# Performance work log

Measured on AMD Instinct MI355X. Metric: run time of the kernel, lower is better.

Reference implementation:

```python
import jax, jax.numpy as jnp
import numpy as np

B, T, C = 2, 4096, 2048
HS = 64
DW, DA, DV, DG = 128, 128, 64, 224


def setup_inputs() -> dict:
    key = jax.random.key(0)
    ks = jax.random.split(key, 32)
    s = 0.02  # small weight scale to keep activations in a sane range
    inp = {
        'x': jax.random.normal(ks[0], (B, T, C), jnp.float32),
        'v_first': jax.random.normal(ks[1], (B, T, C), jnp.float32),
        'x_r': jax.random.uniform(ks[2], (C,), jnp.float32),
        'x_w': jax.random.uniform(ks[3], (C,), jnp.float32),
        'x_k': jax.random.uniform(ks[4], (C,), jnp.float32),
        'x_v': jax.random.uniform(ks[5], (C,), jnp.float32),
        'x_a': jax.random.uniform(ks[6], (C,), jnp.float32),
        'x_g': jax.random.uniform(ks[7], (C,), jnp.float32),
        'w0': jax.random.normal(ks[8], (C,), jnp.float32),
        'w1': jax.random.normal(ks[9], (C, DW), jnp.float32) * s,
        'w2': jax.random.normal(ks[10], (DW, C), jnp.float32) * s,
        'a0': jax.random.normal(ks[11], (C,), jnp.float32),
        'a1': jax.random.normal(ks[12], (C, DA), jnp.float32) * s,
        'a2': jax.random.normal(ks[13], (DA, C), jnp.float32) * s,
        'v0': jax.random.normal(ks[14], (C,), jnp.float32),
        'v1': jax.random.normal(ks[15], (C, DV), jnp.float32) * s,
        'v2': jax.random.normal(ks[16], (DV, C), jnp.float32) * s,
        'g1': jax.random.normal(ks[17], (C, DG), jnp.float32) * s,
        'g2': jax.random.normal(ks[18], (DG, C), jnp.float32) * s,
        'k_k': jax.random.normal(ks[19], (C,), jnp.float32) * 0.1 + 0.71,
        'k_a': jnp.full((C,), 1.02, jnp.float32),
        'Wr': jax.random.normal(ks[20], (C, C), jnp.float32) * s,
        'Wk': jax.random.normal(ks[21], (C, C), jnp.float32) * s,
        'Wv': jax.random.normal(ks[22], (C, C), jnp.float32) * s,
        'head_size': HS,
    }
    return inp


def reference(x, v_first, x_r, x_w, x_k, x_v, x_a, x_g,
              w0, w1, w2, a0, a1, a2, v0, v1, v2, g1, g2,
              k_k, k_a, Wr, Wk, Wv, head_size):
    Bd, Td, Cd = x.shape
    H = Cd // head_size
    # time shift: prepend zero frame, drop last
    xprev = jnp.concatenate([jnp.zeros_like(x[:, :1]), x[:, :-1]], axis=1)
    xx = xprev - x
    xr = x + xx * x_r
    xw = x + xx * x_w
    xk = x + xx * x_k
    xv = x + xx * x_v
    xa = x + xx * x_a
    xg = x + xx * x_g
    r = xr @ Wr.T                                   # [B,T,C]
    w = -jax.nn.softplus(-(w0 + jnp.tanh(xw @ w1) @ w2)) - 0.5
    k = xk @ Wk.T
    v = xv @ Wv.T
    # layer_id = 1 != 0  ->  mix with v_first
    v = v + (v_first - v) * jax.nn.sigmoid(v0 + (xv @ v1) @ v2)
    a = jax.nn.sigmoid(a0 + (xa @ a1) @ a2)
    g = jax.nn.sigmoid(xg @ g1) @ g2
    kk = k * k_k
    kk4 = kk.reshape(Bd, Td, H, head_size)
    nrm = jnp.linalg.norm(kk4, axis=-1, keepdims=True)
    kk = (kk4 / jnp.maximum(nrm, 1e-12)).reshape(Bd, Td, Cd)
    k = k * (1.0 + (a - 1.0) * k_a)
    return (r, w, k, v, a, g, kk, v_first)
```

## Files before the change

### kernel.cpp

```cpp
#include <hip/hip_runtime.h>
#include <hip/hip_bf16.h>

#define MTOT 8192
#define TLEN 4096
#define CDIM 2048
#define SLOT ((size_t)MTOT * CDIM)

typedef __attribute__((ext_vector_type(4))) float f32x4;
typedef __attribute__((ext_vector_type(8))) __bf16 bf16x8;

__device__ __forceinline__ short f2bf(float f) {
  __hip_bfloat16 h = __float2bfloat16(f);
  return __builtin_bit_cast(short, h);
}

__device__ __forceinline__ float sigm(float x) { return 1.f / (1.f + expf(-x)); }

__device__ __forceinline__ void gload16(const void* g, void* l) {
  __builtin_amdgcn_global_load_lds(
      (__attribute__((address_space(1))) void*)g,
      (__attribute__((address_space(3))) void*)l, 16, 0, 0);
}

__device__ __forceinline__ void gemm_core(
    const short* __restrict__ A, int lda,
    const short* __restrict__ Bt, int ldb,
    int K, int m0, int n0,
    short* As, short* Bs, f32x4 acc[4][4])
{
  const int tid  = threadIdx.x;
  const int lane = tid & 63;
  const int wv   = tid >> 6;
  const int wy   = wv >> 1;
  const int wx   = wv & 1;
  const int quad = lane >> 4;
  const int m16  = lane & 15;

  const f32x4 zero = {0.f, 0.f, 0.f, 0.f};
  #pragma unroll
  for (int i = 0; i < 4; ++i)
    #pragma unroll
    for (int j = 0; j < 4; ++j)
      acc[i][j] = zero;

  const int e0 = (wv * 64 + lane) * 8;
  const int e1 = e0 + 2048;
  const int r0 = e0 >> 5, c0 = e0 & 31;
  const int r1 = e1 >> 5, c1 = e1 & 31;
  const int lb0 = wv * 512;
  const int lb1 = 2048 + wv * 512;

  const short* pa0 = A  + (size_t)(m0 + r0) * lda + c0;
  const short* pa1 = A  + (size_t)(m0 + r1) * lda + c1;
  const short* pb0 = Bt + (size_t)(n0 + r0) * ldb + c0;
  const short* pb1 = Bt + (size_t)(n0 + r1) * ldb + c1;

  for (int k0 = 0; k0 < K; k0 += 32) {
    gload16(pa0 + k0, As + lb0);
    gload16(pa1 + k0, As + lb1);
    gload16(pb0 + k0, Bs + lb0);
    gload16(pb1 + k0, Bs + lb1);
    __syncthreads();

    bf16x8 af[4], bfr[4];
    #pragma unroll
    for (int mi = 0; mi < 4; ++mi)
      af[mi] = *(const bf16x8*)(As + (wy*64 + mi*16 + m16)*32 + quad*8);
    #pragma unroll
    for (int ni = 0; ni < 4; ++ni)
      bfr[ni] = *(const bf16x8*)(Bs + (wx*64 + ni*16 + m16)*32 + quad*8);

    #pragma unroll
    for (int mi = 0; mi < 4; ++mi)
      #pragma unroll
      for (int ni = 0; ni < 4; ++ni)
        acc[mi][ni] = __builtin_amdgcn_mfma_f32_16x16x32_bf16(
            af[mi], bfr[ni], acc[mi][ni], 0, 0, 0);
    __syncthreads();
  }
}

__global__ __launch_bounds__(256) void mix_kernel(
    const float* __restrict__ x, const float* __restrict__ vfin,
    const float* __restrict__ cr, const float* __restrict__ cw,
    const float* __restrict__ ck, const float* __restrict__ cv,
    const float* __restrict__ ca, const float* __restrict__ cg,
    short* __restrict__ xr, short* __restrict__ xw, short* __restrict__ xk,
    short* __restrict__ xv, short* __restrict__ xa, short* __restrict__ xg,
    float* __restrict__ vfout)
{
  const size_t i = (size_t)blockIdx.x * 256 + threadIdx.x;
  const size_t e = i * 4;
  const int c = (int)(e & (CDIM - 1));
  const size_t m = e >> 11;
  const int t = (int)(m & (TLEN - 1));
  const float4 xc = *(const float4*)(x + e);
  float4 xp = make_float4(0.f, 0.f, 0.f, 0.f);
  if (t > 0) xp = *(const float4*)(x + e - CDIM);
  const float d0 = xp.x - xc.x, d1 = xp.y - xc.y;
  const float d2 = xp.z - xc.z, d3 = xp.w - xc.w;

  *(float4*)(vfout + e) = *(const float4*)(vfin + e);

  #define EMIT(coef, dst) { \
    const float4 cf = *(const float4*)((coef) + c); \
    short4 s; \
    s.x = f2bf(xc.x + d0 * cf.x); \
    s.y = f2bf(xc.y + d1 * cf.y); \
    s.z = f2bf(xc.z + d2 * cf.z); \
    s.w = f2bf(xc.w + d3 * cf.w); \
    *(short4*)((dst) + e) = s; }
  EMIT(cr, xr) EMIT(cw, xw) EMIT(ck, xk) EMIT(cv, xv) EMIT(ca, xa) EMIT(cg, xg)
  #undef EMIT
}

__global__ __launch_bounds__(256) void cvt_big(
    const float* __restrict__ Wr, const float* __restrict__ Wk,
    const float* __restrict__ Wv,
    short* __restrict__ br, short* __restrict__ bk, short* __restrict__ bv)
{
  const int z = blockIdx.y;
  const float* src = (z == 0) ? Wr : (z == 1) ? Wk : Wv;
  short* dst = (z == 0) ? br : (z == 1) ? bk : bv;
  const size_t e = ((size_t)blockIdx.x * 256 + threadIdx.x) * 4;
  const float4 v = *(const float4*)(src + e);
  short4 s;
  s.x = f2bf(v.x); s.y = f2bf(v.y); s.z = f2bf(v.z); s.w = f2bf(v.w);
  *(short4*)(dst + e) = s;
}

__global__ __launch_bounds__(256) void wtrans(
    const float* __restrict__ w1, const float* __restrict__ a1,
    const float* __restrict__ v1, const float* __restrict__ g1,
    const float* __restrict__ w2, const float* __restrict__ a2,
    const float* __restrict__ v2, const float* __restrict__ g2,
    short* __restrict__ w1t, short* __restrict__ a1t,
    short* __restrict__ v1t, short* __restrict__ g1t,
    short* __restrict__ w2t, short* __restrict__ a2t,
    short* __restrict__ v2t, short* __restrict__ g2t)
{
  const int task = blockIdx.y;
  const int i = blockIdx.x * 256 + threadIdx.x;
  switch (task) {
    case 0: if (i < 128*2048) { int d=i>>11, c=i&2047; w1t[i]=f2bf(w1[(size_t)c*128+d]); } break;
    case 1: if (i < 128*2048) { int d=i>>11, c=i&2047; a1t[i]=f2bf(a1[(size_t)c*128+d]); } break;
    case 2: if (i < 128*2048) { int d=i>>11, c=i&2047; v1t[i]=(d<64)?f2bf(v1[(size_t)c*64+d]):(short)0; } break;
    case 3: if (i < 256*2048) { int d=i>>11, c=i&2047; g1t[i]=(d<224)?f2bf(g1[(size_t)c*224+d]):(short)0; } break;
    case 4: if (i < 2048*128) { int c=i>>7, d=i&127; w2t[i]=f2bf(w2[(size_t)d*2048+c]); } break;
    case 5: if (i < 2048*128) { int c=i>>7, d=i&127; a2t[i]=f2bf(a2[(size_t)d*2048+c]); } break;
    case 6: if (i < 2048*64)  { int c=i>>6, d=i&63;  v2t[i]=f2bf(v2[(size_t)d*2048+c]); } break;
    case 7: if (i < 2048*224) { int c=i/224, d=i-c*224; g2t[i]=f2bf(g2[(size_t)d*2048+c]); } break;
  }
}

__global__ __launch_bounds__(512, 2) void gemm_big2(
    const short* __restrict__ xr, const short* __restrict__ xk,
    const short* __restrict__ xv,
    const short* __restrict__ Wr, const short* __restrict__ Wk,
    const short* __restrict__ Wv,
    float* __restrict__ out)
{
  __shared__ short As[32768];
  __shared__ short Bs[32768];

  const int z = blockIdx.z;
  const short* A  = (z == 0) ? xr : (z == 1) ? xk : xv;
  const short* Bt = (z == 0) ? Wr : (z == 1) ? Wk : Wv;
  float* O = (z == 0) ? out : (z == 1) ? out + 2*SLOT : out + 3*SLOT;

  const int m0 = blockIdx.x * 256, n0 = blockIdx.y * 256;
  const int tid  = threadIdx.x;
  const int lane = tid & 63, wid = tid >> 6;
  const int wm = wid >> 2, wn = wid & 3;
  const int quad = lane >> 4, m16 = lane & 15;

  const int srow = tid >> 2;
  const int csrc = (((tid & 3) ^ ((tid >> 3) & 3)) << 3);
  const size_t aoff = (size_t)(m0 + srow) * CDIM + csrc;
  const size_t boff = (size_t)(n0 + srow) * CDIM + csrc;
  const int lbase = wid * 512;

  const int fslot = ((quad ^ ((m16 >> 1) & 3)) << 3);
  const int abase = (wm*128 + m16) * 32 + fslot;
  const int bbase = (wn*64  + m16) * 32 + fslot;

  f32x4 acc[8][4];
  const f32x4 zf = {0.f, 0.f, 0.f, 0.f};
  #pragma unroll
  for (int i = 0; i < 8; ++i)
    #pragma unroll
    for (int j = 0; j < 4; ++j) acc[i][j] = zf;

  #define STG(REG, BASEP, OFF, KOFF) do { \
    gload16((BASEP) + (OFF) + (KOFF), (REG) + lbase); \
    gload16((BASEP) + (OFF) + (KOFF) + (size_t)128*CDIM, (REG) + lbase + 4096); \
  } while (0)

  STG(As + 0,    A,  aoff, 0);
  STG(Bs + 0,    Bt, boff, 0);
  STG(As + 8192, A,  aoff, 32);
  STG(Bs + 8192, Bt, boff, 32);
  asm volatile("s_waitcnt vmcnt(4)" ::: "memory");
  __builtin_amdgcn_s_barrier();
  __builtin_amdgcn_sched_barrier(0);

  const int NT = CDIM / 64;
  for (int t = 0; t < NT; ++t) {
    const int db = (t & 1) << 14;
    const int nb = 16384 - db;
    const int kn = t*64 + 64;
    const bool pf = (kn < CDIM);
    short* Ar0 = As + db;
    short* Br0 = Bs + db;
    short* Ar1 = As + db + 8192;
    short* Br1 = Bs + db + 8192;

    bf16x8 af[8], b0, b1;

    #pragma unroll
    for (int mi = 0; mi < 8; ++mi)
      af[mi] = *(const bf16x8*)(Ar0 + abase + mi*512);
    b0 = *(const bf16x8*)(Br0 + bbase + 0*512);
    b1 = *(const bf16x8*)(Br0 + bbase + 1*512);
    if (pf) STG(As + nb, A, aoff, kn);
    __builtin_amdgcn_s_barrier();
    asm volatile("s_waitcnt lgkmcnt(0)" ::: "memory");
    __builtin_amdgcn_sched_barrier(0);
    __builtin_amdgcn_s_setprio(1);
    #pragma unroll
    for (int mi = 0; mi < 8; ++mi)
      acc[mi][0] = __builtin_amdgcn_mfma_f32_16x16x32_bf16(af[mi], b0, acc[mi][0], 0, 0, 0);
    #pragma unroll
    for (int mi = 0; mi < 8; ++mi)
      acc[mi][1] = __builtin_amdgcn_mfma_f32_16x16x32_bf16(af[mi], b1, acc[mi][1], 0, 0, 0);
    __builtin_amdgcn_s_setprio(0);
    __builtin_amdgcn_s_barrier();

    b0 = *(const bf16x8*)(Br0 + bbase + 2*512);
    b1 = *(const bf16x8*)(Br0 + bbase + 3*512);
    if (pf) STG(Bs + nb, Bt, boff, kn);
    __builtin_amdgcn_s_barrier();
    asm volatile("s_waitcnt lgkmcnt(0)" ::: "memory");
    __builtin_amdgcn_sched_barrier(0);
    __builtin_amdgcn_s_setprio(1);
    #pragma unroll
    for (int mi = 0; mi < 8; ++mi)
      acc[mi][2] = __builtin_amdgcn_mfma_f32_16x16x32_bf16(af[mi], b0, acc[mi][2], 0, 0, 0);
    #pragma unroll
    for (int mi = 0; mi < 8; ++mi)
      acc[mi][3] = __builtin_amdgcn_mfma_f32_16x16x32_bf16(af[mi], b1, acc[mi][3], 0, 0, 0);
    __builtin_amdgcn_s_setprio(0);
    if (pf) asm volatile("s_waitcnt vmcnt(4)" ::: "memory");
    else    asm volatile("s_waitcnt vmcnt(0)" ::: "memory");
    __builtin_amdgcn_s_barrier();
    __builtin_amdgcn_sched_barrier(0);

    #pragma unroll
    for (int mi = 0; mi < 8; ++mi)
      af[mi] = *(const bf16x8*)(Ar1 + abase + mi*512);
    b0 = *(const bf16x8*)(Br1 + bbase + 0*512);
    b1 = *(const bf16x8*)(Br1 + bbase + 1*512);
    if (pf) STG(As + nb + 8192, A, aoff, kn + 32);
    __builtin_amdgcn_s_barrier();
    asm volatile("s_waitcnt lgkmcnt(0)" ::: "memory");
    __builtin_amdgcn_sched_barrier(0);
    __builtin_amdgcn_s_setprio(1);
    #pragma unroll
    for (int mi = 0; mi < 8; ++mi)
      acc[mi][0] = __builtin_amdgcn_mfma_f32_16x16x32_bf16(af[mi], b0, acc[mi][0], 0, 0, 0);
    #pragma unroll
    for (int mi = 0; mi < 8; ++mi)
      acc[mi][1] = __builtin_amdgcn_mfma_f32_16x16x32_bf16(af[mi], b1, acc[mi][1], 0, 0, 0);
    __builtin_amdgcn_s_setprio(0);
    __builtin_amdgcn_s_barrier();

    b0 = *(const bf16x8*)(Br1 + bbase + 2*512);
    b1 = *(const bf16x8*)(Br1 + bbase + 3*512);
    if (pf) STG(Bs + nb + 8192, Bt, boff, kn + 32);
    __builtin_amdgcn_s_barrier();
    asm volatile("s_waitcnt lgkmcnt(0)" ::: "memory");
    __builtin_amdgcn_sched_barrier(0);
    __builtin_amdgcn_s_setprio(1);
    #pragma unroll
    for (int mi = 0; mi < 8; ++mi)
      acc[mi][2] = __builtin_amdgcn_mfma_f32_16x16x32_bf16(af[mi], b0, acc[mi][2], 0, 0, 0);
    #pragma unroll
    for (int mi = 0; mi < 8; ++mi)
      acc[mi][3] = __builtin_amdgcn_mfma_f32_16x16x32_bf16(af[mi], b1, acc[mi][3], 0, 0, 0);
    __builtin_amdgcn_s_setprio(0);
    asm volatile("s_waitcnt vmcnt(4)" ::: "memory");
    __builtin_amdgcn_s_barrier();
    __builtin_amdgcn_sched_barrier(0);
  }
  #undef STG

  #pragma unroll
  for (int mi = 0; mi < 8; ++mi) {
    const int row = m0 + wm*128 + mi*16 + quad*4;
    #pragma unroll
    for (int ni = 0; ni < 4; ++ni) {
      const int col = n0 + wn*64 + ni*16 + m16;
      #pragma unroll
      for (int r = 0; r < 4; ++r)
        O[(size_t)(row + r) * CDIM + col] = acc[mi][ni][r];
    }
  }
}

__global__ __launch_bounds__(256) void gemm_s1(
    const short* __restrict__ xw, const short* __restrict__ xa,
    const short* __restrict__ xv, const short* __restrict__ xg,
    const short* __restrict__ w1t, const short* __restrict__ a1t,
    const short* __restrict__ v1t, const short* __restrict__ g1t,
    short* __restrict__ hw, short* __restrict__ ha,
    short* __restrict__ hv, short* __restrict__ hg)
{
  const int z = blockIdx.z;
  const int nb = blockIdx.y;
  if (z != 3 && nb != 0) return;
  __shared__ short As[4096], Bs[4096];
  const short* A  = (z==0) ? xw  : (z==1) ? xa  : (z==2) ? xv  : xg;
  const short* Bt = (z==0) ? w1t : (z==1) ? a1t : (z==2) ? v1t : g1t;
  short* H        = (z==0) ? hw  : (z==1) ? ha  : (z==2) ? hv  : hg;
  const int Nreal = (z==2) ? 64 : (z==3) ? 224 : 128;
  const int m0 = blockIdx.x * 128, n0 = nb * 128;
  f32x4 acc[4][4];
  gemm_core(A, CDIM, Bt, CDIM, CDIM, m0, n0, As, Bs, acc);

  const int tid=threadIdx.x, lane=tid&63, wv=tid>>6;
  const int wy=wv>>1, wx=wv&1, quad=lane>>4, m16=lane&15;
  #pragma unroll
  for (int mi = 0; mi < 4; ++mi) {
    const int mb = m0 + wy*64 + mi*16 + quad*4;
    #pragma unroll
    for (int ni = 0; ni < 4; ++ni) {
      const int n = n0 + wx*64 + ni*16 + m16;
      if (n < Nreal) {
        #pragma unroll
        for (int r = 0; r < 4; ++r) {
          float v = acc[mi][ni][r];
          if (z == 0) v = tanhf(v);
          else if (z == 3) v = sigm(v);
          H[(size_t)(mb + r) * Nreal + n] = f2bf(v);
        }
      }
    }
  }
}

__global__ __launch_bounds__(256) void gemm_s2(
    const short* __restrict__ hw, const short* __restrict__ ha,
    const short* __restrict__ hv, const short* __restrict__ hg,
    const short* __restrict__ w2t, const short* __restrict__ a2t,
    const short* __restrict__ v2t, const short* __restrict__ g2t,
    const float* __restrict__ w0, const float* __restrict__ a0,
    const float* __restrict__ v0, const float* __restrict__ vfirst,
    float* __restrict__ out)
{
  __shared__ short As[4096], Bs[4096];
  const int z = blockIdx.z;
  const short* A  = (z==0) ? hw  : (z==1) ? ha  : (z==2) ? hv  : hg;
  const short* Bt = (z==0) ? w2t : (z==1) ? a2t : (z==2) ? v2t : g2t;
  const int K = (z==2) ? 64 : (z==3) ? 224 : 128;
  const int m0 = blockIdx.x * 128, n0 = blockIdx.y * 128;
  f32x4 acc[4][4];
  gemm_core(A, K, Bt, K, K, m0, n0, As, Bs, acc);

  const int tid=threadIdx.x, lane=tid&63, wv=tid>>6;
  const int wy=wv>>1, wx=wv&1, quad=lane>>4, m16=lane&15;
  #pragma unroll
  for (int mi = 0; mi < 4; ++mi) {
    const int mb = m0 + wy*64 + mi*16 + quad*4;
    #pragma unroll
    for (int ni = 0; ni < 4; ++ni) {
      const int n = n0 + wx*64 + ni*16 + m16;
      #pragma unroll
      for (int r = 0; r < 4; ++r) {
        const float val = acc[mi][ni][r];
        const size_t idx = (size_t)(mb + r) * CDIM + n;
        if (z == 0) {
          float zz = w0[n] + val;
          float sp = fmaxf(-zz, 0.f) + log1pf(expf(-fabsf(zz)));
          out[SLOT + idx] = -sp - 0.5f;
        } else if (z == 1) {
          out[4*SLOT + idx] = sigm(a0[n] + val);
        } else if (z == 2) {
          const float gate = sigm(v0[n] + val);
          const float vr = out[3*SLOT + idx];
          out[3*SLOT + idx] = vr + (vfirst[idx] - vr) * gate;
        } else {
          out[5*SLOT + idx] = val;
        }
      }
    }
  }
}

__global__ __launch_bounds__(256) void fin_k(
    const float* __restrict__ kkc, const float* __restrict__ kac,
    float* __restrict__ out)
{
  const int wid  = blockIdx.x * 4 + (threadIdx.x >> 6);
  const int lane = threadIdx.x & 63;
  const size_t m = (size_t)(wid >> 5);
  const int h = wid & 31;
  const int c = h * 64 + lane;
  const size_t idx = m * CDIM + c;
  const float kraw = out[2*SLOT + idx];
  const float a    = out[4*SLOT + idx];
  const float kkv  = kraw * kkc[c];
  float ss = kkv * kkv;
  #pragma unroll
  for (int o = 32; o >= 1; o >>= 1) ss += __shfl_xor(ss, o, 64);
  const float nrm = sqrtf(ss);
  out[6*SLOT + idx] = kkv / fmaxf(nrm, 1e-12f);
  out[2*SLOT + idx] = kraw * (1.f + (a - 1.f) * kac[c]);
}

extern "C" void kernel_launch(void* const* d_in, const int* in_sizes, int n_in,
                              void* d_out, int out_size, void* d_ws, size_t ws_size,
                              hipStream_t stream) {
  (void)in_sizes; (void)n_in; (void)out_size; (void)ws_size;
  const float* x   = (const float*)d_in[0];
  const float* vf  = (const float*)d_in[1];
  const float* x_r = (const float*)d_in[2];
  const float* x_w = (const float*)d_in[3];
  const float* x_k = (const float*)d_in[4];
  const float* x_v = (const float*)d_in[5];
  const float* x_a = (const float*)d_in[6];
  const float* x_g = (const float*)d_in[7];
  const float* w0  = (const float*)d_in[8];
  const float* w1  = (const float*)d_in[9];
  const float* w2  = (const float*)d_in[10];
  const float* a0  = (const float*)d_in[11];
  const float* a1  = (const float*)d_in[12];
  const float* a2  = (const float*)d_in[13];
  const float* v0  = (const float*)d_in[14];
  const float* v1  = (const float*)d_in[15];
  const float* v2  = (const float*)d_in[16];
  const float* g1  = (const float*)d_in[17];
  const float* g2  = (const float*)d_in[18];
  const float* k_k = (const float*)d_in[19];
  const float* k_a = (const float*)d_in[20];
  const float* Wr  = (const float*)d_in[21];
  const float* Wk  = (const float*)d_in[22];
  const float* Wv  = (const float*)d_in[23];

  float* out = (float*)d_out;

  short* xr_b = (short*)(out + 1*SLOT);
  short* xw_b = xr_b + SLOT;
  short* xk_b = (short*)(out + 4*SLOT);
  short* xv_b = xk_b + SLOT;
  short* xa_b = (short*)(out + 5*SLOT);
  short* xg_b = xa_b + SLOT;

  char* wsp = (char*)d_ws;
  size_t off = 0;
  #define ALLOC(var, bytes) short* var = (short*)(wsp + off); off += (((size_t)(bytes)) + 255) & ~(size_t)255;
  ALLOC(Wr_b, (size_t)CDIM*CDIM*2)
  ALLOC(Wk_b, (size_t)CDIM*CDIM*2)
  ALLOC(Wv_b, (size_t)CDIM*CDIM*2)
  ALLOC(w1t, 128*2048*2)
  ALLOC(a1t, 128*2048*2)
  ALLOC(v1t, 128*2048*2)
  ALLOC(g1t, 256*2048*2)
  ALLOC(w2t, 2048*128*2)
  ALLOC(a2t, 2048*128*2)
  ALLOC(v2t, 2048*64*2)
  ALLOC(g2t, 2048*224*2)
  ALLOC(hw, (size_t)MTOT*128*2)
  ALLOC(ha, (size_t)MTOT*128*2)
  ALLOC(hv, (size_t)MTOT*64*2)
  ALLOC(hg, (size_t)MTOT*224*2)
  #undef ALLOC

  mix_kernel<<<dim3(16384), 256, 0, stream>>>(
      x, vf, x_r, x_w, x_k, x_v, x_a, x_g,
      xr_b, xw_b, xk_b, xv_b, xa_b, xg_b, out + 7*SLOT);

  cvt_big<<<dim3(4096, 3), 256, 0, stream>>>(Wr, Wk, Wv, Wr_b, Wk_b, Wv_b);

  wtrans<<<dim3(2048, 8), 256, 0, stream>>>(
      w1, a1, v1, g1, w2, a2, v2, g2,
      w1t, a1t, v1t, g1t, w2t, a2t, v2t, g2t);

  gemm_big2<<<dim3(32, 8, 3), 512, 0, stream>>>(
      xr_b, xk_b, xv_b, Wr_b, Wk_b, Wv_b, out);

  gemm_s1<<<dim3(64, 2, 4), 256, 0, stream>>>(
      xw_b, xa_b, xv_b, xg_b, w1t, a1t, v1t, g1t, hw, ha, hv, hg);

  gemm_s2<<<dim3(64, 16, 4), 256, 0, stream>>>(
      hw, ha, hv, hg, w2t, a2t, v2t, g2t, w0, a0, v0, vf, out);

  fin_k<<<dim3(65536), 256, 0, stream>>>(k_k, k_a, out);
}
```

Measured before the change: 1.276 ms.

## Merge prep kernels, fold small GEMMs into big GEMM grid, fuse finalize into epilogue

Combines the mix, weight-convert and weight-transpose kernels into one launch. The first-stage low-rank GEMMs run as an extra z-slice of the big GEMM grid, with two 256-thread sub-tiles per 512-thread block. The k normalization and k/a finalize is fused into the gemm_s2 epilogue for the a-branch, which removes the fin_k pass over memory. The big GEMM also loads all four B fragments up front to cut LDS waits, and its tile index is remapped. The cost is more register pressure and heavier mixed-role blocks.

```diff
diff --git a/kernel.cpp b/kernel.cpp
--- a/kernel.cpp
+++ b/kernel.cpp
@@ -23,12 +23,12 @@
 }
 
 __device__ __forceinline__ void gemm_core(
+    int tid,
     const short* __restrict__ A, int lda,
     const short* __restrict__ Bt, int ldb,
     int K, int m0, int n0,
     short* As, short* Bs, f32x4 acc[4][4])
 {
-  const int tid  = threadIdx.x;
   const int lane = tid & 63;
   const int wv   = tid >> 6;
   const int wy   = wv >> 1;
@@ -80,76 +80,78 @@
   }
 }
 
-__global__ __launch_bounds__(256) void mix_kernel(
+__global__ __launch_bounds__(256) void front(
     const float* __restrict__ x, const float* __restrict__ vfin,
     const float* __restrict__ cr, const float* __restrict__ cw,
     const float* __restrict__ ck, const float* __restrict__ cv,
     const float* __restrict__ ca, const float* __restrict__ cg,
-    short* __restrict__ xr, short* __restrict__ xw, short* __restrict__ xk,
-    short* __restrict__ xv, short* __restrict__ xa, short* __restrict__ xg,
-    float* __restrict__ vfout)
-{
-  const size_t i = (size_t)blockIdx.x * 256 + threadIdx.x;
-  const size_t e = i * 4;
-  const int c = (int)(e & (CDIM - 1));
-  const size_t m = e >> 11;
-  const int t = (int)(m & (TLEN - 1));
-  const float4 xc = *(const float4*)(x + e);
-  float4 xp = make_float4(0.f, 0.f, 0.f, 0.f);
-  if (t > 0) xp = *(const float4*)(x + e - CDIM);
-  const float d0 = xp.x - xc.x, d1 = xp.y - xc.y;
-  const float d2 = xp.z - xc.z, d3 = xp.w - xc.w;
-
-  *(float4*)(vfout + e) = *(const float4*)(vfin + e);
-
-  #define EMIT(coef, dst) { \
-    const float4 cf = *(const float4*)((coef) + c); \
-    short4 s; \
-    s.x = f2bf(xc.x + d0 * cf.x); \
-    s.y = f2bf(xc.y + d1 * cf.y); \
-    s.z = f2bf(xc.z + d2 * cf.z); \
-    s.w = f2bf(xc.w + d3 * cf.w); \
-    *(short4*)((dst) + e) = s; }
-  EMIT(cr, xr) EMIT(cw, xw) EMIT(ck, xk) EMIT(cv, xv) EMIT(ca, xa) EMIT(cg, xg)
-  #undef EMIT
-}
-
-__global__ __launch_bounds__(256) void cvt_big(
     const float* __restrict__ Wr, const float* __restrict__ Wk,
     const float* __restrict__ Wv,
-    short* __restrict__ br, short* __restrict__ bk, short* __restrict__ bv)
-{
-  const int z = blockIdx.y;
-  const float* src = (z == 0) ? Wr : (z == 1) ? Wk : Wv;
-  short* dst = (z == 0) ? br : (z == 1) ? bk : bv;
-  const size_t e = ((size_t)blockIdx.x * 256 + threadIdx.x) * 4;
-  const float4 v = *(const float4*)(src + e);
-  short4 s;
-  s.x = f2bf(v.x); s.y = f2bf(v.y); s.z = f2bf(v.z); s.w = f2bf(v.w);
-  *(short4*)(dst + e) = s;
-}
-
-__global__ __launch_bounds__(256) void wtrans(
     const float* __restrict__ w1, const float* __restrict__ a1,
     const float* __restrict__ v1, const float* __restrict__ g1,
     const float* __restrict__ w2, const float* __restrict__ a2,
     const float* __restrict__ v2, const float* __restrict__ g2,
+    short* __restrict__ xr, short* __restrict__ xw, short* __restrict__ xk,
+    short* __restrict__ xv, short* __restrict__ xa, short* __restrict__ xg,
+    float* __restrict__ vfout,
+    short* __restrict__ Wrb, short* __restrict__ Wkb, short* __restrict__ Wvb,
     short* __restrict__ w1t, short* __restrict__ a1t,
     short* __restrict__ v1t, short* __restrict__ g1t,
     short* __restrict__ w2t, short* __restrict__ a2t,
     short* __restrict__ v2t, short* __restrict__ g2t)
 {
-  const int task = blockIdx.y;
-  const int i = blockIdx.x * 256 + threadIdx.x;
-  switch (task) {
-    case 0: if (i < 128*2048) { int d=i>>11, c=i&2047; w1t[i]=f2bf(w1[(size_t)c*128+d]); } break;
-    case 1: if (i < 128*2048) { int d=i>>11, c=i&2047; a1t[i]=f2bf(a1[(size_t)c*128+d]); } break;
-    case 2: if (i < 128*2048) { int d=i>>11, c=i&2047; v1t[i]=(d<64)?f2bf(v1[(size_t)c*64+d]):(short)0; } break;
-    case 3: if (i < 256*2048) { int d=i>>11, c=i&2047; g1t[i]=(d<224)?f2bf(g1[(size_t)c*224+d]):(short)0; } break;
-    case 4: if (i < 2048*128) { int c=i>>7, d=i&127; w2t[i]=f2bf(w2[(size_t)d*2048+c]); } break;
-    case 5: if (i < 2048*128) { int c=i>>7, d=i&127; a2t[i]=f2bf(a2[(size_t)d*2048+c]); } break;
-    case 6: if (i < 2048*64)  { int c=i>>6, d=i&63;  v2t[i]=f2bf(v2[(size_t)d*2048+c]); } break;
-    case 7: if (i < 2048*224) { int c=i/224, d=i-c*224; g2t[i]=f2bf(g2[(size_t)d*2048+c]); } break;
+  const int b = blockIdx.x;
+  const int tidx = threadIdx.x;
+
+  if (b < 16384) {
+    const size_t i = (size_t)b * 256 + tidx;
+    const size_t e = i * 4;
+    const int c = (int)(e & (CDIM - 1));
+    const size_t m = e >> 11;
+    const int t = (int)(m & (TLEN - 1));
+    const float4 xc = *(const float4*)(x + e);
+    float4 xp = make_float4(0.f, 0.f, 0.f, 0.f);
+    if (t > 0) xp = *(const float4*)(x + e - CDIM);
+    const float d0 = xp.x - xc.x, d1 = xp.y - xc.y;
+    const float d2 = xp.z - xc.z, d3 = xp.w - xc.w;
+
+    *(float4*)(vfout + e) = *(const float4*)(vfin + e);
+
+    #define EMIT(coef, dst) { \
+      const float4 cf = *(const float4*)((coef) + c); \
+      short4 s; \
+      s.x = f2bf(xc.x + d0 * cf.x); \
+      s.y = f2bf(xc.y + d1 * cf.y); \
+      s.z = f2bf(xc.z + d2 * cf.z); \
+      s.w = f2bf(xc.w + d3 * cf.w); \
+      *(short4*)((dst) + e) = s; }
+    EMIT(cr, xr) EMIT(cw, xw) EMIT(ck, xk) EMIT(cv, xv) EMIT(ca, xa) EMIT(cg, xg)
+    #undef EMIT
+  } else if (b < 28672) {
+    const int lb = b - 16384;
+    const int z = lb >> 12;
+    const int xb = lb & 4095;
+    const float* src = (z == 0) ? Wr : (z == 1) ? Wk : Wv;
+    short* dst = (z == 0) ? Wrb : (z == 1) ? Wkb : Wvb;
+    const size_t e = ((size_t)xb * 256 + tidx) * 4;
+    const float4 v = *(const float4*)(src + e);
+    short4 s;
+    s.x = f2bf(v.x); s.y = f2bf(v.y); s.z = f2bf(v.z); s.w = f2bf(v.w);
+    *(short4*)(dst + e) = s;
+  } else {
+    const int lb = b - 28672;
+    const int task = lb >> 11;
+    const int i = (lb & 2047) * 256 + tidx;
+    switch (task) {
+      case 0: if (i < 128*2048) { int d=i>>11, c=i&2047; w1t[i]=f2bf(w1[(size_t)c*128+d]); } break;
+      case 1: if (i < 128*2048) { int d=i>>11, c=i&2047; a1t[i]=f2bf(a1[(size_t)c*128+d]); } break;
+      case 2: if (i < 128*2048) { int d=i>>11, c=i&2047; v1t[i]=(d<64)?f2bf(v1[(size_t)c*64+d]):(short)0; } break;
+      case 3: if (i < 256*2048) { int d=i>>11, c=i&2047; g1t[i]=(d<224)?f2bf(g1[(size_t)c*224+d]):(short)0; } break;
+      case 4: if (i < 2048*128) { int c=i>>7, d=i&127; w2t[i]=f2bf(w2[(size_t)d*2048+c]); } break;
+      case 5: if (i < 2048*128) { int c=i>>7, d=i&127; a2t[i]=f2bf(a2[(size_t)d*2048+c]); } break;
+      case 6: if (i < 2048*64)  { int c=i>>6, d=i&63;  v2t[i]=f2bf(v2[(size_t)d*2048+c]); } break;
+      case 7: if (i < 2048*224) { int c=i/224, d=i-c*224; g2t[i]=f2bf(g2[(size_t)d*2048+c]); } break;
+    }
   }
 }
 
@@ -158,17 +160,67 @@
     const short* __restrict__ xv,
     const short* __restrict__ Wr, const short* __restrict__ Wk,
     const short* __restrict__ Wv,
+    const short* __restrict__ xw, const short* __restrict__ xa,
+    const short* __restrict__ xg,
+    const short* __restrict__ w1t, const short* __restrict__ a1t,
+    const short* __restrict__ v1t, const short* __restrict__ g1t,
+    short* __restrict__ hw, short* __restrict__ ha,
+    short* __restrict__ hv, short* __restrict__ hg,
     float* __restrict__ out)
 {
   __shared__ short As[32768];
   __shared__ short Bs[32768];
 
   const int z = blockIdx.z;
+
+  if (z == 3) {
+    const int flat = blockIdx.x + (blockIdx.y << 5);
+    if (flat >= 160) return;
+    const int sub = threadIdx.x >> 8;
+    const int tid = threadIdx.x & 255;
+    const int tile = flat * 2 + sub;
+    const int t = tile >> 6;
+    const int mt = tile & 63;
+    const short* A1 = (t==0) ? xw  : (t==1) ? xa  : (t==2) ? xv  : xg;
+    const short* B1 = (t==0) ? w1t : (t==1) ? a1t : (t==2) ? v1t : g1t;
+    short* H        = (t==0) ? hw  : (t==1) ? ha  : (t==2) ? hv  : hg;
+    const int Nreal = (t==2) ? 64 : (t>=3) ? 224 : 128;
+    const int n0 = (t==4) ? 128 : 0;
+    const int m0 = mt * 128;
+    short* sA = As + sub * 8192;
+    short* sB = sA + 4096;
+    f32x4 acc[4][4];
+    gemm_core(tid, A1, CDIM, B1, CDIM, CDIM, m0, n0, sA, sB, acc);
+
+    const int lane=tid&63, wv=tid>>6;
+    const int wy=wv>>1, wx=wv&1, quad=lane>>4, m16=lane&15;
+    #pragma unroll
+    for (int mi = 0; mi < 4; ++mi) {
+      const int mb = m0 + wy*64 + mi*16 + quad*4;
+      #pragma unroll
+      for (int ni = 0; ni < 4; ++ni) {
+        const int n = n0 + wx*64 + ni*16 + m16;
+        if (n < Nreal) {
+          #pragma unroll
+          for (int r = 0; r < 4; ++r) {
+            float v = acc[mi][ni][r];
+            if (t == 0) v = tanhf(v);
+            else if (t >= 3) v = sigm(v);
+            H[(size_t)(mb + r) * Nreal + n] = f2bf(v);
+          }
+        }
+      }
+    }
+    return;
+  }
+
   const short* A  = (z == 0) ? xr : (z == 1) ? xk : xv;
   const short* Bt = (z == 0) ? Wr : (z == 1) ? Wk : Wv;
   float* O = (z == 0) ? out : (z == 1) ? out + 2*SLOT : out + 3*SLOT;
 
-  const int m0 = blockIdx.x * 256, n0 = blockIdx.y * 256;
+  const int flat = blockIdx.x + (blockIdx.y << 5);
+  const int m0 = (flat >> 3) * 256;
+  const int n0 = (flat & 7)  * 256;
   const int tid  = threadIdx.x;
   const int lane = tid & 63, wid = tid >> 6;
   const int wm = wid >> 2, wn = wid & 3;
@@ -215,13 +267,15 @@
     short* Ar1 = As + db + 8192;
     short* Br1 = Bs + db + 8192;
 
-    bf16x8 af[8], b0, b1;
+    bf16x8 af[8], b0, b1, b2, b3;
 
     #pragma unroll
     for (int mi = 0; mi < 8; ++mi)
       af[mi] = *(const bf16x8*)(Ar0 + abase + mi*512);
     b0 = *(const bf16x8*)(Br0 + bbase + 0*512);
     b1 = *(const bf16x8*)(Br0 + bbase + 1*512);
+    b2 = *(const bf16x8*)(Br0 + bbase + 2*512);
+    b3 = *(const bf16x8*)(Br0 + bbase + 3*512);
     if (pf) STG(As + nb, A, aoff, kn);
     __builtin_amdgcn_s_barrier();
     asm volatile("s_waitcnt lgkmcnt(0)" ::: "memory");
@@ -236,37 +290,35 @@
     __builtin_amdgcn_s_setprio(0);
     __builtin_amdgcn_s_barrier();
 
-    b0 = *(const bf16x8*)(Br0 + bbase + 2*512);
-    b1 = *(const bf16x8*)(Br0 + bbase + 3*512);
     if (pf) STG(Bs + nb, Bt, boff, kn);
+    __builtin_amdgcn_s_barrier();
+    __builtin_amdgcn_s_setprio(1);
+    #pragma unroll
+    for (int mi = 0; mi < 8; ++mi)
+      acc[mi][2] = __builtin_amdgcn_mfma_f32_16x16x32_bf16(af[mi], b2, acc[mi][2], 0, 0, 0);
+    #pragma unroll
+    for (int mi = 0; mi < 8; ++mi)
+      acc[mi][3] = __builtin_amdgcn_mfma_f32_16x16x32_bf16(af[mi], b3, acc[mi][3], 0, 0, 0);
+    __builtin_amdgcn_s_setprio(0);
+    if (pf) asm volatile("s_waitcnt vmcnt(4)" ::: "memory");
+    else    asm volatile("s_waitcnt vmcnt(0)" ::: "memory");
+    __builtin_amdgcn_s_barrier();
+    __builtin_amdgcn_sched_barrier(0);
+
+    #pragma unroll
+    for (int mi = 0; mi < 8; ++mi)
+      af[mi] = *(const bf16x8*)(Ar1 + abase + mi*512);
+    b0 = *(const bf16x8*)(Br1 + bbase + 0*512);
+    b1 = *(const bf16x8*)(Br1 + bbase + 1*512);
+    b2 = *(const bf16x8*)(Br1 + bbase + 2*512);
+    b3 = *(const bf16x8*)(Br1 + bbase + 3*512);
+    if (pf) STG(As + nb + 8192, A, aoff, kn + 32);
     __builtin_amdgcn_s_barrier();
     asm volatile("s_waitcnt lgkmcnt(0)" ::: "memory");
     __builtin_amdgcn_sched_barrier(0);
     __builtin_amdgcn_s_setprio(1);
     #pragma unroll
     for (int mi = 0; mi < 8; ++mi)
-      acc[mi][2] = __builtin_amdgcn_mfma_f32_16x16x32_bf16(af[mi], b0, acc[mi][2], 0, 0, 0);
-    #pragma unroll
-    for (int mi = 0; mi < 8; ++mi)
-      acc[mi][3] = __builtin_amdgcn_mfma_f32_16x16x32_bf16(af[mi], b1, acc[mi][3], 0, 0, 0);
-    __builtin_amdgcn_s_setprio(0);
-    if (pf) asm volatile("s_waitcnt vmcnt(4)" ::: "memory");
-    else    asm volatile("s_waitcnt vmcnt(0)" ::: "memory");
-    __builtin_amdgcn_s_barrier();
-    __builtin_amdgcn_sched_barrier(0);
-
-    #pragma unroll
-    for (int mi = 0; mi < 8; ++mi)
-      af[mi] = *(const bf16x8*)(Ar1 + abase + mi*512);
-    b0 = *(const bf16x8*)(Br1 + bbase + 0*512);
-    b1 = *(const bf16x8*)(Br1 + bbase + 1*512);
-    if (pf) STG(As + nb + 8192, A, aoff, kn + 32);
-    __builtin_amdgcn_s_barrier();
-    asm volatile("s_waitcnt lgkmcnt(0)" ::: "memory");
-    __builtin_amdgcn_sched_barrier(0);
-    __builtin_amdgcn_s_setprio(1);
-    #pragma unroll
-    for (int mi = 0; mi < 8; ++mi)
       acc[mi][0] = __builtin_amdgcn_mfma_f32_16x16x32_bf16(af[mi], b0, acc[mi][0], 0, 0, 0);
     #pragma unroll
     for (int mi = 0; mi < 8; ++mi)
@@ -274,19 +326,15 @@
     __builtin_amdgcn_s_setprio(0);
     __builtin_amdgcn_s_barrier();
 
-    b0 = *(const bf16x8*)(Br1 + bbase + 2*512);
-    b1 = *(const bf16x8*)(Br1 + bbase + 3*512);
     if (pf) STG(Bs + nb + 8192, Bt, boff, kn + 32);
     __builtin_amdgcn_s_barrier();
-    asm volatile("s_waitcnt lgkmcnt(0)" ::: "memory");
-    __builtin_amdgcn_sched_barrier(0);
     __builtin_amdgcn_s_setprio(1);
     #pragma unroll
     for (int mi = 0; mi < 8; ++mi)
-      acc[mi][2] = __builtin_amdgcn_mfma_f32_16x16x32_bf16(af[mi], b0, acc[mi][2], 0, 0, 0);
-    #pragma unroll
-    for (int mi = 0; mi < 8; ++mi)
-      acc[mi][3] = __builtin_amdgcn_mfma_f32_16x16x32_bf16(af[mi], b1, acc[mi][3], 0, 0, 0);
+      acc[mi][2] = __builtin_amdgcn_mfma_f32_16x16x32_bf16(af[mi], b2, acc[mi][2], 0, 0, 0);
+    #pragma unroll
+    for (int mi = 0; mi < 8; ++mi)
+      acc[mi][3] = __builtin_amdgcn_mfma_f32_16x16x32_bf16(af[mi], b3, acc[mi][3], 0, 0, 0);
     __builtin_amdgcn_s_setprio(0);
     asm volatile("s_waitcnt vmcnt(4)" ::: "memory");
     __builtin_amdgcn_s_barrier();
@@ -307,47 +355,6 @@
   }
 }
 
-__global__ __launch_bounds__(256) void gemm_s1(
-    const short* __restrict__ xw, const short* __restrict__ xa,
-    const short* __restrict__ xv, const short* __restrict__ xg,
-    const short* __restrict__ w1t, const short* __restrict__ a1t,
-    const short* __restrict__ v1t, const short* __restrict__ g1t,
-    short* __restrict__ hw, short* __restrict__ ha,
-    short* __restrict__ hv, short* __restrict__ hg)
-{
-  const int z = blockIdx.z;
-  const int nb = blockIdx.y;
-  if (z != 3 && nb != 0) return;
-  __shared__ short As[4096], Bs[4096];
-  const short* A  = (z==0) ? xw  : (z==1) ? xa  : (z==2) ? xv  : xg;
-  const short* Bt = (z==0) ? w1t : (z==1) ? a1t : (z==2) ? v1t : g1t;
-  short* H        = (z==0) ? hw  : (z==1) ? ha  : (z==2) ? hv  : hg;
-  const int Nreal = (z==2) ? 64 : (z==3) ? 224 : 128;
-  const int m0 = blockIdx.x * 128, n0 = nb * 128;
-  f32x4 acc[4][4];
-  gemm_core(A, CDIM, Bt, CDIM, CDIM, m0, n0, As, Bs, acc);
-
-  const int tid=threadIdx.x, lane=tid&63, wv=tid>>6;
-  const int wy=wv>>1, wx=wv&1, quad=lane>>4, m16=lane&15;
-  #pragma unroll
-  for (int mi = 0; mi < 4; ++mi) {
-    const int mb = m0 + wy*64 + mi*16 + quad*4;
-    #pragma unroll
-    for (int ni = 0; ni < 4; ++ni) {
-      const int n = n0 + wx*64 + ni*16 + m16;
-      if (n < Nreal) {
-        #pragma unroll
-        for (int r = 0; r < 4; ++r) {
-          float v = acc[mi][ni][r];
-          if (z == 0) v = tanhf(v);
-          else if (z == 3) v = sigm(v);
-          H[(size_t)(mb + r) * Nreal + n] = f2bf(v);
-        }
-      }
-    }
-  }
-}
-
 __global__ __launch_bounds__(256) void gemm_s2(
     const short* __restrict__ hw, const short* __restrict__ ha,
     const short* __restrict__ hv, const short* __restrict__ hg,
@@ -355,6 +362,7 @@
     const short* __restrict__ v2t, const short* __restrict__ g2t,
     const float* __restrict__ w0, const float* __restrict__ a0,
     const float* __restrict__ v0, const float* __restrict__ vfirst,
+    const float* __restrict__ kkc, const float* __restrict__ kac,
     float* __restrict__ out)
 {
   __shared__ short As[4096], Bs[4096];
@@ -364,57 +372,64 @@
   const int K = (z==2) ? 64 : (z==3) ? 224 : 128;
   const int m0 = blockIdx.x * 128, n0 = blockIdx.y * 128;
   f32x4 acc[4][4];
-  gemm_core(A, K, Bt, K, K, m0, n0, As, Bs, acc);
+  gemm_core(threadIdx.x, A, K, Bt, K, K, m0, n0, As, Bs, acc);
 
   const int tid=threadIdx.x, lane=tid&63, wv=tid>>6;
   const int wy=wv>>1, wx=wv&1, quad=lane>>4, m16=lane&15;
   #pragma unroll
   for (int mi = 0; mi < 4; ++mi) {
     const int mb = m0 + wy*64 + mi*16 + quad*4;
-    #pragma unroll
-    for (int ni = 0; ni < 4; ++ni) {
-      const int n = n0 + wx*64 + ni*16 + m16;
+    if (z == 1) {
       #pragma unroll
       for (int r = 0; r < 4; ++r) {
-        const float val = acc[mi][ni][r];
-        const size_t idx = (size_t)(mb + r) * CDIM + n;
-        if (z == 0) {
-          float zz = w0[n] + val;
-          float sp = fmaxf(-zz, 0.f) + log1pf(expf(-fabsf(zz)));
-          out[SLOT + idx] = -sp - 0.5f;
-        } else if (z == 1) {
-          out[4*SLOT + idx] = sigm(a0[n] + val);
-        } else if (z == 2) {
-          const float gate = sigm(v0[n] + val);
-          const float vr = out[3*SLOT + idx];
-          out[3*SLOT + idx] = vr + (vfirst[idx] - vr) * gate;
-        } else {
-          out[5*SLOT + idx] = val;
+        float av[4], kr[4], kkv[4];
+        float ss = 0.f;
+        #pragma unroll
+        for (int ni = 0; ni < 4; ++ni) {
+          const int n = n0 + wx*64 + ni*16 + m16;
+          const size_t idx = (size_t)(mb + r) * CDIM + n;
+          av[ni] = sigm(a0[n] + acc[mi][ni][r]);
+          kr[ni] = out[2*SLOT + idx];
+          kkv[ni] = kr[ni] * kkc[n];
+          ss += kkv[ni] * kkv[ni];
+        }
+        ss += __shfl_xor(ss, 1, 64);
+        ss += __shfl_xor(ss, 2, 64);
+        ss += __shfl_xor(ss, 4, 64);
+        ss += __shfl_xor(ss, 8, 64);
+        const float inv = 1.f / fmaxf(sqrtf(ss), 1e-12f);
+        #pragma unroll
+        for (int ni = 0; ni < 4; ++ni) {
+          const int n = n0 + wx*64 + ni*16 + m16;
+          const size_t idx = (size_t)(mb + r) * CDIM + n;
+          out[4*SLOT + idx] = av[ni];
+          out[2*SLOT + idx] = kr[ni] * (1.f + (av[ni] - 1.f) * kac[n]);
+          out[6*SLOT + idx] = kkv[ni] * inv;
+        }
+      }
+    } else {
+      #pragma unroll
+      for (int ni = 0; ni < 4; ++ni) {
+        const int n = n0 + wx*64 + ni*16 + m16;
+        #pragma unroll
+        for (int r = 0; r < 4; ++r) {
+          const float val = acc[mi][ni][r];
+          const size_t idx = (size_t)(mb + r) * CDIM + n;
+          if (z == 0) {
+            float zz = w0[n] + val;
+            float sp = fmaxf(-zz, 0.f) + log1pf(expf(-fabsf(zz)));
+            out[SLOT + idx] = -sp - 0.5f;
+          } else if (z == 2) {
+            const float gate = sigm(v0[n] + val);
+            const float vr = out[3*SLOT + idx];
+            out[3*SLOT + idx] = vr + (vfirst[idx] - vr) * gate;
+          } else {
+            out[5*SLOT + idx] = val;
+          }
         }
       }
     }
   }
-}
-
-__global__ __launch_bounds__(256) void fin_k(
-    const float* __restrict__ kkc, const float* __restrict__ kac,
-    float* __restrict__ out)
-{
-  const int wid  = blockIdx.x * 4 + (threadIdx.x >> 6);
-  const int lane = threadIdx.x & 63;
-  const size_t m = (size_t)(wid >> 5);
-  const int h = wid & 31;
-  const int c = h * 64 + lane;
-  const size_t idx = m * CDIM + c;
-  const float kraw = out[2*SLOT + idx];
-  const float a    = out[4*SLOT + idx];
-  const float kkv  = kraw * kkc[c];
-  float ss = kkv * kkv;
-  #pragma unroll
-  for (int o = 32; o >= 1; o >>= 1) ss += __shfl_xor(ss, o, 64);
-  const float nrm = sqrtf(ss);
-  out[6*SLOT + idx] = kkv / fmaxf(nrm, 1e-12f);
-  out[2*SLOT + idx] = kraw * (1.f + (a - 1.f) * kac[c]);
 }
 
 extern "C" void kernel_launch(void* const* d_in, const int* in_sizes, int n_in,
@@ -475,24 +490,17 @@
   ALLOC(hg, (size_t)MTOT*224*2)
   #undef ALLOC
 
-  mix_kernel<<<dim3(16384), 256, 0, stream>>>(
+  front<<<dim3(45056), 256, 0, stream>>>(
       x, vf, x_r, x_w, x_k, x_v, x_a, x_g,
-      xr_b, xw_b, xk_b, xv_b, xa_b, xg_b, out + 7*SLOT);
-
-  cvt_big<<<dim3(4096, 3), 256, 0, stream>>>(Wr, Wk, Wv, Wr_b, Wk_b, Wv_b);
-
-  wtrans<<<dim3(2048, 8), 256, 0, stream>>>(
-      w1, a1, v1, g1, w2, a2, v2, g2,
-      w1t, a1t, v1t, g1t, w2t, a2t, v2t, g2t);
-
-  gemm_big2<<<dim3(32, 8, 3), 512, 0, stream>>>(
-      xr_b, xk_b, xv_b, Wr_b, Wk_b, Wv_b, out);
-
-  gemm_s1<<<dim3(64, 2, 4), 256, 0, stream>>>(
-      xw_b, xa_b, xv_b, xg_b, w1t, a1t, v1t, g1t, hw, ha, hv, hg);
+      Wr, Wk, Wv, w1, a1, v1, g1, w2, a2, v2, g2,
+      xr_b, xw_b, xk_b, xv_b, xa_b, xg_b, out + 7*SLOT,
+      Wr_b, Wk_b, Wv_b, w1t, a1t, v1t, g1t, w2t, a2t, v2t, g2t);
+
+  gemm_big2<<<dim3(32, 8, 4), 512, 0, stream>>>(
+      xr_b, xk_b, xv_b, Wr_b, Wk_b, Wv_b,
+      xw_b, xa_b, xg_b, w1t, a1t, v1t, g1t,
+      hw, ha, hv, hg, out);
 
   gemm_s2<<<dim3(64, 16, 4), 256, 0, stream>>>(
-      hw, ha, hv, hg, w2t, a2t, v2t, g2t, w0, a0, v0, vf, out);
-
-  fin_k<<<dim3(65536), 256, 0, stream>>>(k_k, k_a, out);
-}
+      hw, ha, hv, hg, w2t, a2t, v2t, g2t, w0, a0, v0, vf, k_k, k_a, out);
+}
```

New measurement: 1.246 ms. 1.02x faster.
